# Optimization experiments

Hardware: AMD Instinct MI355X
Metric: run time of the kernel (lower is better)

The kernel has to match this reference:

```python
import jax, jax.numpy as jnp
import numpy as np

N_QUBITS = 8


def _zsign(n):
    # sign of PauliZ eigenvalue for each basis state on each wire; wire 0 is MSB
    idx = np.arange(2 ** n)
    bits = (idx[:, None] >> (n - 1 - np.arange(n))) & 1
    return jnp.asarray(1.0 - 2.0 * bits, dtype=jnp.float32)  # (2^n, n)


ZSIGN = _zsign(N_QUBITS)


def qgate(angles):
    """Simulate: RX(angle_w) per wire (encoder RX + trainable RX already summed,
    since RX(a)RX(b)=RX(a+b)), CNOT chain, then <Z_w> per wire.
    angles: (B, n) real -> (B, n) expectation values in [-1, 1]."""
    B, n = angles.shape
    c = jnp.cos(angles / 2).astype(jnp.complex64)
    s = (-1j * jnp.sin(angles / 2)).astype(jnp.complex64)
    # product state |psi> = kron_w [cos(a/2), -i sin(a/2)], wire 0 = MSB
    state = jnp.ones((B, 1), jnp.complex64)
    for w in range(n):
        qs = jnp.stack([c[:, w], s[:, w]], axis=-1)  # (B, 2)
        state = (state[:, :, None] * qs[:, None, :]).reshape(B, -1)
    # CNOT chain on wires (i, i+1)
    for i in range(n - 1):
        d0, d1 = 2 ** i, 2 ** (n - i - 2)
        st = state.reshape(B, d0, 2, 2, d1)
        st = jnp.stack([st[:, :, 0], st[:, :, 1, ::-1]], axis=2)
        state = st.reshape(B, -1)
    probs = state.real ** 2 + state.imag ** 2  # (B, 2^n)
    return probs @ ZSIGN  # (B, n)


def setup_inputs() -> dict:
    key = jax.random.key(0)
    S, B, D, H = 256, 256, 256, N_QUBITS
    fan = D + H
    ks = jax.random.split(key, 13)
    inputs = jax.random.normal(ks[0], (S, B, D), dtype=jnp.float32)
    hx = jnp.zeros((B, H), jnp.float32)
    cx = jnp.zeros((B, H), jnp.float32)
    bound = 1.0 / np.sqrt(fan)

    def lin(kw, kb):
        W = jax.random.uniform(kw, (H, fan), minval=-bound, maxval=bound, dtype=jnp.float32)
        b = jax.random.uniform(kb, (H,), minval=-bound, maxval=bound, dtype=jnp.float32)
        return W, b

    Wf, bf = lin(ks[1], ks[2])
    Wi, bi = lin(ks[3], ks[4])
    Wu, bu = lin(ks[5], ks[6])
    Wo, bo = lin(ks[7], ks[8])
    theta_f = jax.random.normal(ks[9], (H,), dtype=jnp.float32) * 0.1
    theta_i = jax.random.normal(ks[10], (H,), dtype=jnp.float32) * 0.1
    theta_u = jax.random.normal(ks[11], (H,), dtype=jnp.float32) * 0.1
    theta_o = jax.random.normal(ks[12], (H,), dtype=jnp.float32) * 0.1
    return {"inputs": inputs, "hx": hx, "cx": cx,
            "Wf": Wf, "bf": bf, "Wi": Wi, "bi": bi,
            "Wu": Wu, "bu": bu, "Wo": Wo, "bo": bo,
            "theta_f": theta_f, "theta_i": theta_i,
            "theta_u": theta_u, "theta_o": theta_o}


def reference(inputs, hx, cx, Wf, bf, Wi, bi, Wu, bu, Wo, bo,
              theta_f, theta_i, theta_u, theta_o):
    def step(carry, x):
        h, c = carry
        z = jnp.concatenate([x, h], axis=1)  # (B, D+H)
        f = jax.nn.sigmoid(qgate(z @ Wf.T + bf + theta_f))
        i = jax.nn.sigmoid(qgate(z @ Wi.T + bi + theta_i))
        g = jnp.tanh(qgate(z @ Wu.T + bu + theta_u))
        o = jax.nn.sigmoid(qgate(z @ Wo.T + bo + theta_o))
        c = f * c + i * g
        h = o * jnp.tanh(c)
        return (h, c), h

    (hT, cT), outs = jax.lax.scan(step, (hx, cx), inputs)
    return outs, hT, cT
```

## Files before the change

kernel.cpp:

```cpp
#include <hip/hip_runtime.h>


#define S_LEN 256
#define BATCH 256
#define DIMK  256
#define FAN   264
#define NROWS (S_LEN * BATCH)
#define WS_NEED ((size_t)NROWS * 32 * 4)

typedef __attribute__((address_space(1))) const void GV;
typedef __attribute__((address_space(3))) void LV;

__device__ __forceinline__ float lo16f(unsigned u) {
    union { unsigned u; float f; } v; v.u = u << 16; return v.f;
}
__device__ __forceinline__ float hi16f(unsigned u) {
    union { unsigned u; float f; } v; v.u = u & 0xffff0000u; return v.f;
}
__device__ __forceinline__ float b2f(unsigned short u) {
    union { unsigned u; float f; } v; v.u = ((unsigned)u) << 16; return v.f;
}
__device__ __forceinline__ unsigned short f2b(float f) {
    union { float f; unsigned u; } v; v.f = f;
    unsigned r = v.u + 0x7fffu + ((v.u >> 16) & 1u);
    return (unsigned short)(r >> 16);
}
__device__ __forceinline__ float sane(float x) {
    return (__builtin_fabsf(x) < 1e30f) ? x : 0.f;
}
__device__ __forceinline__ float ldE(const void* p, int idx, bool f32) {
    return f32 ? ((const float*)p)[idx] : b2f(((const unsigned short*)p)[idx]);
}
__device__ __forceinline__ void stE(void* p, long idx, float v, bool f32) {
    if (f32) ((float*)p)[idx] = v;
    else     ((unsigned short*)p)[idx] = f2b(v);
}
__device__ __forceinline__ float sigp(float x) {
    float x2 = x * x;
    float p = fmaf(x2, 0.0026216f, -0.0217557f);
    p = fmaf(x2, p, 0.250193f);
    return fmaf(x, p, 0.5f);
}
__device__ __forceinline__ float tanh_pade(float x) {
    float x2 = x * x;
    float num = x * fmaf(x2, x2 + 105.f, 945.f);
    float den = fmaf(x2, fmaf(x2, 15.f, 420.f), 945.f);
    return __fdividef(num, den);
}
__device__ __forceinline__ float tanh_f(float x) {
    return 1.f - __fdividef(2.f, __expf(2.f * x) + 1.f);
}

template<int CTRL>
__device__ __forceinline__ float dpp_f(float x) {
    int xi = __builtin_bit_cast(int, x);
    int r = __builtin_amdgcn_update_dpp(xi, xi, CTRL, 0xF, 0xF, false);
    return __builtin_bit_cast(float, r);
}
template<int IMM>
__device__ __forceinline__ float swz_f(float x) {
    return __builtin_bit_cast(float,
        __builtin_amdgcn_ds_swizzle(__builtin_bit_cast(int, x), IMM));
}
__device__ __forceinline__ float rdlane_f(float x, int l) {
    return __builtin_bit_cast(float,
        __builtin_amdgcn_readlane(__builtin_bit_cast(int, x), l));
}

__device__ __forceinline__ int sniff_f32(const void* X) {
    const unsigned short* u = (const unsigned short*)X;
    int hits = 0;
    for (int i = 0; i < 64; ++i) {
        int e = (u[2 * i] >> 7) & 0xFF;
        if (e >= 110 && e <= 135) ++hits;
    }
    return (hits < 32) ? 1 : 0;
}

__global__ __launch_bounds__(512, 4) void qlstm_gemm(
    const void* __restrict__ X,
    const void* __restrict__ Wf, const void* __restrict__ Wi,
    const void* __restrict__ Wu, const void* __restrict__ Wo,
    const void* __restrict__ bf_, const void* __restrict__ bi_,
    const void* __restrict__ bu_, const void* __restrict__ bo_,
    const void* __restrict__ tf, const void* __restrict__ ti,
    const void* __restrict__ tu, const void* __restrict__ to_,
    float* __restrict__ A)
{
    __shared__ float Xs[8][32][32];
    __shared__ float red[8][32][32];

    const int tid = threadIdx.x;
    const bool f32 = sniff_f32(X) != 0;

    const int kv = tid >> 6;
    const int l  = tid & 63;
    const int o  = l & 31;
    const int th = l >> 5;
    const int g  = o >> 3, w = o & 7;
    const void* Wg = (g == 0) ? Wf : (g == 1) ? Wi : (g == 2) ? Wu : Wo;
    const void* bg_[4] = { bf_, bi_, bu_, bo_ };
    const void* tg_[4] = { tf, ti, tu, to_ };

    float4 wreg[8];
    if (f32) {
        const float4* wr = (const float4*)((const float*)Wg + w * FAN + kv * 32);
#pragma unroll
        for (int i = 0; i < 8; ++i) wreg[i] = wr[i];
    } else {
        const uint4* wr = (const uint4*)((const unsigned short*)Wg + w * FAN + kv * 32);
#pragma unroll
        for (int i = 0; i < 4; ++i) {
            uint4 wu = wr[i];
            wreg[2 * i + 0] = make_float4(lo16f(wu.x), hi16f(wu.x),
                                          lo16f(wu.y), hi16f(wu.y));
            wreg[2 * i + 1] = make_float4(lo16f(wu.z), hi16f(wu.z),
                                          lo16f(wu.w), hi16f(wu.w));
        }
    }

    const long rowbase = (long)blockIdx.x * 64;

    for (int chunk = 0; chunk < 2; ++chunk) {
        if (f32) {
#pragma unroll
            for (int i = 0; i < 4; ++i) {
                const long row = rowbase + chunk * 32 + i * 8 + (l >> 3);
                const int t = (int)(row & 255), bb = (int)(row >> 8);
                const float* src = (const float*)X
                        + ((long)t * BATCH + bb) * DIMK + kv * 32 + (l & 7) * 4;
                __builtin_amdgcn_global_load_lds((GV*)src,
                        (LV*)&Xs[kv][i * 8][0], 16, 0, 0);
            }
            asm volatile("s_waitcnt vmcnt(0)" ::: "memory");
            for (int j = 0; j < 16; ++j) {
                const int r = th * 16 + j;
                const float4* xv = (const float4*)&Xs[kv][r][0];
                float a0 = 0.f, a1 = 0.f, a2 = 0.f, a3 = 0.f;
#pragma unroll
                for (int i = 0; i < 8; ++i) {
                    float4 xu = xv[i];
                    a0 = fmaf(xu.x, wreg[i].x, a0);
                    a1 = fmaf(xu.y, wreg[i].y, a1);
                    a2 = fmaf(xu.z, wreg[i].z, a2);
                    a3 = fmaf(xu.w, wreg[i].w, a3);
                }
                red[kv][r][o] = (a0 + a1) + (a2 + a3);
            }
        } else {
            for (int j = 0; j < 16; ++j) {
                const int r = th * 16 + j;
                const long row = rowbase + chunk * 32 + r;
                const int t = (int)(row & 255), bb = (int)(row >> 8);
                const uint4* xr = (const uint4*)((const unsigned short*)X
                        + ((long)t * BATCH + bb) * DIMK + kv * 32);
                float a0 = 0.f, a1 = 0.f, a2 = 0.f, a3 = 0.f;
#pragma unroll
                for (int i = 0; i < 4; ++i) {
                    uint4 xu = xr[i];
                    a0 = fmaf(lo16f(xu.x), wreg[2 * i].x, a0);
                    a1 = fmaf(hi16f(xu.x), wreg[2 * i].y, a1);
                    a2 = fmaf(lo16f(xu.y), wreg[2 * i].z, a2);
                    a3 = fmaf(hi16f(xu.y), wreg[2 * i].w, a3);
                    a0 = fmaf(lo16f(xu.z), wreg[2 * i + 1].x, a0);
                    a1 = fmaf(hi16f(xu.z), wreg[2 * i + 1].y, a1);
                    a2 = fmaf(lo16f(xu.w), wreg[2 * i + 1].z, a2);
                    a3 = fmaf(hi16f(xu.w), wreg[2 * i + 1].w, a3);
                }
                red[kv][r][o] = (a0 + a1) + (a2 + a3);
            }
        }
        __syncthreads();
        for (int idx = tid; idx < 32 * 32; idx += 512) {
            const int rl = idx >> 5, oo = idx & 31;
            float s = 0.f;
#pragma unroll
            for (int k = 0; k < 8; ++k) s += red[k][rl][oo];
            const int g2 = oo >> 3, w2 = oo & 7;
            const float bt = sane(ldE(bg_[g2], w2, f32))
                           + sane(ldE(tg_[g2], w2, f32));
            A[(rowbase + chunk * 32 + rl) * 32 + w2 * 4 + g2] = sane(s) + bt;
        }
        __syncthreads();
    }
}

__global__ __launch_bounds__(64) void qlstm_rec(
    const void* __restrict__ X,  const void* __restrict__ hx, const void* __restrict__ cx,
    const void* __restrict__ Wf, const void* __restrict__ Wi,
    const void* __restrict__ Wu, const void* __restrict__ Wo,
    void* __restrict__ out, const float* __restrict__ A)
{
    __shared__ float4 Abuf[2][2048];

    const int tid = threadIdx.x;
    const bool f32 = sniff_f32(X) != 0;

    const int p     = tid & 15;
    const int w     = p & 7;
    const int half  = p >> 3;
    const int bsub  = tid >> 4;
    const int bglob = blockIdx.x * 4 + bsub;

    const void* WgA = half ? Wu : Wf;
    const void* WgB = half ? Wo : Wi;

    float WhA[8], WhB[8];
#pragma unroll
    for (int m = 0; m < 8; ++m) {
        WhA[m] = sane(ldE(WgA, w * FAN + DIMK + (w ^ m), f32));
        WhB[m] = sane(ldE(WgB, w * FAN + DIMK + (w ^ m), f32));
    }
    const float d3 = half ? -0.028402f : 0.f;
    const float d2 = half ?  0.121713f : 0.0026216f;
    const float d1 = half ? -0.331717f : -0.0217557f;
    const float d0 = half ?  1.0f      : 0.250193f;
    const float s0 = half ?  0.f       : 0.5f;

    float h = sane(ldE(hx, bglob * 8 + w, f32));
    float c = sane(ldE(cx, bglob * 8 + w, f32));

    auto cumprod8 = [&](float e) {
        { float v = dpp_f<0x111>(e); e = (w >= 1) ? e * v : e; }
        { float v = dpp_f<0x112>(e); e = (w >= 2) ? e * v : e; }
        { float v = dpp_f<0x114>(e); e = (w >= 4) ? e * v : e; }
        return e;
    };

    const float4* A4 = (const float4*)A;
    const int w2 = tid & 7, bs = (tid >> 3) & 3, tl0 = tid >> 5;
    const float4* srcb = A4
        + ((((long)(blockIdx.x * 4 + bs)) << 8 | tl0) << 3) + w2;
    auto stage = [&](int ch, int bufi) {
        const float4* s0p = srcb + ((long)ch << 9);
#pragma unroll
        for (int i = 0; i < 32; ++i) {
            __builtin_amdgcn_global_load_lds((GV*)(s0p + (i << 4)),
                                             (LV*)&Abuf[bufi][i << 6], 16, 0, 0);
        }
    };

    auto STEP = [&](int t, float aA, float aB) {
        float h0 = h;
        float h1 = dpp_f<0xB1>(h);
        float h2 = dpp_f<0x4E>(h);
        float h3 = dpp_f<0xB1>(h2);
        float h7 = dpp_f<0x141>(h);
        float h6 = dpp_f<0xB1>(h7);
        float h5 = dpp_f<0x4E>(h7);
        float h4 = dpp_f<0xB1>(h5);

        float e0, e1;
        {
            float a = fmaf(h0, WhA[0], aA), b = h1 * WhA[1];
            a = fmaf(h2, WhA[2], a); b = fmaf(h3, WhA[3], b);
            a = fmaf(h4, WhA[4], a); b = fmaf(h5, WhA[5], b);
            a = fmaf(h6, WhA[6], a); b = fmaf(h7, WhA[7], b);
            e0 = a + b;
            a = fmaf(h0, WhB[0], aB); b = h1 * WhB[1];
            a = fmaf(h2, WhB[2], a); b = fmaf(h3, WhB[3], b);
            a = fmaf(h4, WhB[4], a); b = fmaf(h5, WhB[5], b);
            a = fmaf(h6, WhB[6], a); b = fmaf(h7, WhB[7], b);
            e1 = a + b;
        }
        float EA = cumprod8(__cosf(e0));
        float EB = cumprod8(__cosf(e1));
        float x2 = EA * EA;
        float pp = fmaf(x2, d3, d2);
        pp = fmaf(x2, pp, d1);
        pp = fmaf(x2, pp, d0);
        float vA = fmaf(EA, pp, s0);
        float vB = sigp(EB);
        float rA = dpp_f<0x128>(vA);
        float rB = dpp_f<0x128>(vB);
        float vf = half ? rA : vA;
        float vi = half ? rB : vB;
        float vu = half ? vA : rA;
        float vo = half ? vB : rB;
        c = fmaf(vf, c, vi * vu);
        h = vo * tanh_pade(c);
        if (half == 0)
            stE(out, (long)t * 2048 + bglob * 8 + w, h, f32);
    };

    stage(0, 0);
    asm volatile("s_waitcnt vmcnt(0)" ::: "memory");

    const float2* Ab2 = (const float2*)&Abuf[0][0];
    const int rdbase = (bsub * 8 + w) * 2 + half;
    for (int ch = 0; ch < 4; ++ch) {
        const int cb = ch & 1;
        if (ch + 1 < 4) stage(ch + 1, cb ^ 1);
#pragma unroll 4
        for (int s = 0; s < 64; ++s) {
            float2 a = Ab2[cb * 4096 + s * 64 + rdbase];
            STEP(ch * 64 + s, a.x, a.y);
        }
        asm volatile("s_waitcnt vmcnt(0)" ::: "memory");
    }
    if (half == 0) {
        stE(out, 524288L + bglob * 8 + w, h, f32);
        stE(out, 526336L + bglob * 8 + w, c, f32);
    }
}

__global__ __launch_bounds__(320, 1) void qlstm_fused_v6(
    const void* __restrict__ X,  const void* __restrict__ hx, const void* __restrict__ cx,
    const void* __restrict__ Wf, const void* __restrict__ bf_,
    const void* __restrict__ Wi, const void* __restrict__ bi_,
    const void* __restrict__ Wu, const void* __restrict__ bu_,
    const void* __restrict__ Wo, const void* __restrict__ bo_,
    const void* __restrict__ tf, const void* __restrict__ ti,
    const void* __restrict__ tu, const void* __restrict__ to_,
    void* __restrict__ out)
{
    __shared__ float As4[2][4][32][32];

    const int tid = threadIdx.x;
    const int b   = blockIdx.x;
    const bool f32 = sniff_f32(X) != 0;

    const int wv   = tid >> 6;
    const int lane = tid & 63;
    const int kv   = wv - 1;
    const int o    = lane & 31;
    const int th   = lane >> 5;
    const int g    = o >> 3, w = o & 7;
    const void* Wg = (g == 0) ? Wf : (g == 1) ? Wi : (g == 2) ? Wu : Wo;

    float4 wreg[16];
    if (wv >= 1) {
        if (f32) {
            const float4* wr = (const float4*)((const float*)Wg + w * FAN + kv * 64);
#pragma unroll
            for (int i = 0; i < 16; ++i) wreg[i] = wr[i];
        } else {
            const uint4* wr = (const uint4*)((const unsigned short*)Wg + w * FAN + kv * 64);
#pragma unroll
            for (int i = 0; i < 8; ++i) {
                uint4 wu = wr[i];
                wreg[2 * i + 0] = make_float4(lo16f(wu.x), hi16f(wu.x),
                                              lo16f(wu.y), hi16f(wu.y));
                wreg[2 * i + 1] = make_float4(lo16f(wu.z), hi16f(wu.z),
                                              lo16f(wu.w), hi16f(wu.w));
            }
        }
    }

    auto fill = [&](int ch) {
        float (*dst)[32] = As4[ch & 1][kv];
        const int tb = ch * 32 + th * 16;
        if (f32) {
            for (int j = 0; j < 16; ++j) {
                const float4* xr = (const float4*)((const float*)X
                        + ((long)(tb + j) * BATCH + b) * DIMK + kv * 64);
                float a0 = 0.f, a1 = 0.f, a2 = 0.f, a3 = 0.f;
#pragma unroll
                for (int i = 0; i < 16; ++i) {
                    float4 xu = xr[i];
                    a0 = fmaf(xu.x, wreg[i].x, a0);
                    a1 = fmaf(xu.y, wreg[i].y, a1);
                    a2 = fmaf(xu.z, wreg[i].z, a2);
                    a3 = fmaf(xu.w, wreg[i].w, a3);
                }
                dst[th * 16 + j][o] = sane((a0 + a1) + (a2 + a3));
            }
        } else {
            for (int j = 0; j < 16; ++j) {
                const uint4* xr = (const uint4*)((const unsigned short*)X
                        + ((long)(tb + j) * BATCH + b) * DIMK + kv * 64);
                float a0 = 0.f, a1 = 0.f, a2 = 0.f, a3 = 0.f;
#pragma unroll
                for (int i = 0; i < 8; ++i) {
                    uint4 xu = xr[i];
                    a0 = fmaf(lo16f(xu.x), wreg[2 * i].x, a0);
                    a1 = fmaf(hi16f(xu.x), wreg[2 * i].y, a1);
                    a2 = fmaf(lo16f(xu.y), wreg[2 * i].z, a2);
                    a3 = fmaf(hi16f(xu.y), wreg[2 * i].w, a3);
                    a0 = fmaf(lo16f(xu.z), wreg[2 * i + 1].x, a0);
                    a1 = fmaf(hi16f(xu.z), wreg[2 * i + 1].y, a1);
                    a2 = fmaf(lo16f(xu.w), wreg[2 * i + 1].z, a2);
                    a3 = fmaf(hi16f(xu.w), wreg[2 * i + 1].w, a3);
                }
                dst[th * 16 + j][o] = sane((a0 + a1) + (a2 + a3));
            }
        }
    };

    float Wh[8];
    float bt = 0.f, h = 0.f, c = 0.f, qv = 1.f;
    int rw = 0, rg = 0;
    if (tid < 32) {
        rw = tid & 7; rg = tid >> 3;
        const void* bg = (rg == 0) ? bf_ : (rg == 1) ? bi_ : (rg == 2) ? bu_ : bo_;
        const void* tg = (rg == 0) ? tf  : (rg == 1) ? ti  : (rg == 2) ? tu  : to_;
        const int wr = rw * FAN;
#pragma unroll
        for (int j = 0; j < 8; ++j)
            Wh[j] = sane(ldE(Wg, wr + DIMK + j, f32));
        bt = sane(ldE(bg, rw, f32)) + sane(ldE(tg, rw, f32));
        h  = sane(ldE(hx, b * 8 + rw, f32));
        c  = sane(ldE(cx, b * 8 + rw, f32));
        qv = (rg == 2) ? 2.f : 1.f;
    }
    if (wv == 0) __builtin_amdgcn_s_setprio(1);

    if (wv >= 1) fill(0);
    __syncthreads();

    for (int ch = 0; ch < 8; ++ch) {
        if (wv >= 1 && ch + 1 < 8) fill(ch + 1);
        if (tid < 32) {
            const int buf = ch & 1;
            float n0 = As4[buf][0][0][tid], n1 = As4[buf][1][0][tid];
            float n2 = As4[buf][2][0][tid], n3 = As4[buf][3][0][tid];
            float a_cur = (n0 + n1) + (n2 + n3);
            for (int s = 0; s < 32; ++s) {
                const int sn = (s < 31) ? s + 1 : s;
                float m0 = As4[buf][0][sn][tid], m1 = As4[buf][1][sn][tid];
                float m2 = As4[buf][2][sn][tid], m3 = As4[buf][3][sn][tid];
                float dd0 = 0.f, dd1 = 0.f;
#pragma unroll
                for (int j = 0; j < 8; j += 2) {
                    dd0 = fmaf(rdlane_f(h, j),     Wh[j],     dd0);
                    dd1 = fmaf(rdlane_f(h, j + 1), Wh[j + 1], dd1);
                }
                float ang = a_cur + bt + (dd0 + dd1);
                float e = __cosf(ang);
                { float v = dpp_f<0x111>(e); e = (rw >= 1) ? e * v : e; }
                { float v = dpp_f<0x112>(e); e = (rw >= 2) ? e * v : e; }
                { float v = dpp_f<0x114>(e); e = (rw >= 4) ? e * v : e; }
                float ez  = __expf(qv * e);
                float val = 1.f - __fdividef(qv, ez + 1.f);
                float fg = swz_f<0x007>(val);
                float ig = swz_f<0x107>(val);
                float ug = swz_f<0x207>(val);
                float og = swz_f<0x307>(val);
                c = fmaf(fg, c, ig * ug);
                float e2 = __expf(2.f * c);
                float th2 = 1.f - __fdividef(2.f, e2 + 1.f);
                h = og * th2;
                if (rg == 0)
                    stE(out, (long)(ch * 32 + s) * 2048 + b * 8 + rw, h, f32);
                a_cur = (m0 + m1) + (m2 + m3);
            }
        }
        __syncthreads();
    }

    if (tid < 32 && rg == 0) {
        stE(out, 524288L + b * 8 + rw, h, f32);
        stE(out, 526336L + b * 8 + rw, c, f32);
    }
}

extern "C" void kernel_launch(void* const* d_in, const int* in_sizes, int n_in,
                              void* d_out, int out_size, void* d_ws, size_t ws_size,
                              hipStream_t stream) {
    if (d_ws != nullptr && ws_size >= WS_NEED) {
        qlstm_gemm<<<dim3(NROWS / 64), dim3(512), 0, stream>>>(
            d_in[0], d_in[3], d_in[5], d_in[7], d_in[9],
            d_in[4], d_in[6], d_in[8], d_in[10],
            d_in[11], d_in[12], d_in[13], d_in[14],
            (float*)d_ws);
        qlstm_rec<<<dim3(BATCH / 4), dim3(64), 0, stream>>>(
            d_in[0], d_in[1], d_in[2],
            d_in[3], d_in[5], d_in[7], d_in[9],
            d_out, (const float*)d_ws);
    } else {
        qlstm_fused_v6<<<dim3(BATCH), dim3(320), 0, stream>>>(
            d_in[0], d_in[1], d_in[2],
            d_in[3], d_in[4], d_in[5], d_in[6],
            d_in[7], d_in[8], d_in[9], d_in[10],
            d_in[11], d_in[12], d_in[13], d_in[14],
            d_out);
    }
}
```

Measured before the change: 207.2 us.

## Restructure gemm register tiling and split recurrent gates across lanes

The input-projection GEMM now holds all four gate weight slices in registers per thread, so each X row loaded from LDS is reused across the four gates, and both chunks are staged up front as a double buffer. The recurrent kernel assigns one gate per lane (2 batches per wave instead of 4) and exchanges gate values through DPP and ds_swizzle, which halves the per-lane serial work in each time step and doubles the number of blocks. The cost is higher register pressure in the GEMM (its occupancy hint drops from 4 to 2) and extra cross-lane shuffles in the recurrence.

```diff
diff --git a/kernel.cpp b/kernel.cpp
--- a/kernel.cpp
+++ b/kernel.cpp
@@ -35,20 +35,20 @@
     if (f32) ((float*)p)[idx] = v;
     else     ((unsigned short*)p)[idx] = f2b(v);
 }
+__device__ __forceinline__ float tanh_pade(float x) {
+    float x2 = x * x;
+    float num = x * fmaf(x2, x2 + 105.f, 945.f);
+    float den = fmaf(x2, fmaf(x2, 15.f, 420.f), 945.f);
+    return __fdividef(num, den);
+}
+__device__ __forceinline__ float tanh_f(float x) {
+    return 1.f - __fdividef(2.f, __expf(2.f * x) + 1.f);
+}
 __device__ __forceinline__ float sigp(float x) {
     float x2 = x * x;
     float p = fmaf(x2, 0.0026216f, -0.0217557f);
     p = fmaf(x2, p, 0.250193f);
     return fmaf(x, p, 0.5f);
-}
-__device__ __forceinline__ float tanh_pade(float x) {
-    float x2 = x * x;
-    float num = x * fmaf(x2, x2 + 105.f, 945.f);
-    float den = fmaf(x2, fmaf(x2, 15.f, 420.f), 945.f);
-    return __fdividef(num, den);
-}
-__device__ __forceinline__ float tanh_f(float x) {
-    return 1.f - __fdividef(2.f, __expf(2.f * x) + 1.f);
 }
 
 template<int CTRL>
@@ -77,7 +77,7 @@
     return (hits < 32) ? 1 : 0;
 }
 
-__global__ __launch_bounds__(512, 4) void qlstm_gemm(
+__global__ __launch_bounds__(512, 2) void qlstm_gemm(
     const void* __restrict__ X,
     const void* __restrict__ Wf, const void* __restrict__ Wi,
     const void* __restrict__ Wu, const void* __restrict__ Wo,
@@ -87,90 +87,75 @@
     const void* __restrict__ tu, const void* __restrict__ to_,
     float* __restrict__ A)
 {
-    __shared__ float Xs[8][32][32];
+    __shared__ float Xs[2][8][32][32];
     __shared__ float red[8][32][32];
 
     const int tid = threadIdx.x;
     const bool f32 = sniff_f32(X) != 0;
 
-    const int kv = tid >> 6;
-    const int l  = tid & 63;
-    const int o  = l & 31;
-    const int th = l >> 5;
-    const int g  = o >> 3, w = o & 7;
-    const void* Wg = (g == 0) ? Wf : (g == 1) ? Wi : (g == 2) ? Wu : Wo;
+    const int kv  = tid >> 6;
+    const int l   = tid & 63;
+    const int o4  = l & 7;
+    const int rg8 = l >> 3;
+    const void* Wq[4] = { Wf, Wi, Wu, Wo };
     const void* bg_[4] = { bf_, bi_, bu_, bo_ };
     const void* tg_[4] = { tf, ti, tu, to_ };
 
-    float4 wreg[8];
-    if (f32) {
-        const float4* wr = (const float4*)((const float*)Wg + w * FAN + kv * 32);
-#pragma unroll
-        for (int i = 0; i < 8; ++i) wreg[i] = wr[i];
-    } else {
-        const uint4* wr = (const uint4*)((const unsigned short*)Wg + w * FAN + kv * 32);
+    float4 wregQ[4][8];
+#pragma unroll
+    for (int q = 0; q < 4; ++q) {
+        if (f32) {
+            const float4* wr = (const float4*)((const float*)Wq[q] + o4 * FAN + kv * 32);
+#pragma unroll
+            for (int i = 0; i < 8; ++i) wregQ[q][i] = wr[i];
+        } else {
+            const uint4* wr = (const uint4*)((const unsigned short*)Wq[q] + o4 * FAN + kv * 32);
+#pragma unroll
+            for (int i = 0; i < 4; ++i) {
+                uint4 wu = wr[i];
+                wregQ[q][2 * i + 0] = make_float4(lo16f(wu.x), hi16f(wu.x),
+                                                  lo16f(wu.y), hi16f(wu.y));
+                wregQ[q][2 * i + 1] = make_float4(lo16f(wu.z), hi16f(wu.z),
+                                                  lo16f(wu.w), hi16f(wu.w));
+            }
+        }
+    }
+
+    const long rowbase = (long)blockIdx.x * 64;
+
+    auto stageX = [&](int chunk, int cbuf) {
 #pragma unroll
         for (int i = 0; i < 4; ++i) {
-            uint4 wu = wr[i];
-            wreg[2 * i + 0] = make_float4(lo16f(wu.x), hi16f(wu.x),
-                                          lo16f(wu.y), hi16f(wu.y));
-            wreg[2 * i + 1] = make_float4(lo16f(wu.z), hi16f(wu.z),
-                                          lo16f(wu.w), hi16f(wu.w));
-        }
-    }
-
-    const long rowbase = (long)blockIdx.x * 64;
-
-    for (int chunk = 0; chunk < 2; ++chunk) {
-        if (f32) {
-#pragma unroll
-            for (int i = 0; i < 4; ++i) {
-                const long row = rowbase + chunk * 32 + i * 8 + (l >> 3);
-                const int t = (int)(row & 255), bb = (int)(row >> 8);
-                const float* src = (const float*)X
-                        + ((long)t * BATCH + bb) * DIMK + kv * 32 + (l & 7) * 4;
-                __builtin_amdgcn_global_load_lds((GV*)src,
-                        (LV*)&Xs[kv][i * 8][0], 16, 0, 0);
-            }
-            asm volatile("s_waitcnt vmcnt(0)" ::: "memory");
-            for (int j = 0; j < 16; ++j) {
-                const int r = th * 16 + j;
-                const float4* xv = (const float4*)&Xs[kv][r][0];
+            const long row = rowbase + chunk * 32 + i * 8 + (l >> 3);
+            const int t = (int)(row & 255), bb = (int)(row >> 8);
+            const float* src = (const float*)X
+                    + ((long)t * BATCH + bb) * DIMK + kv * 32 + (l & 7) * 4;
+            __builtin_amdgcn_global_load_lds((GV*)src,
+                    (LV*)&Xs[cbuf][kv][i * 8][0], 16, 0, 0);
+        }
+    };
+    auto computeChunk = [&](int cbuf) {
+        for (int j = 0; j < 4; ++j) {
+            const int r = rg8 * 4 + j;
+            const float4* xv = (const float4*)&Xs[cbuf][kv][r][0];
+            float4 x8[8];
+#pragma unroll
+            for (int i = 0; i < 8; ++i) x8[i] = xv[i];
+#pragma unroll
+            for (int q = 0; q < 4; ++q) {
                 float a0 = 0.f, a1 = 0.f, a2 = 0.f, a3 = 0.f;
 #pragma unroll
                 for (int i = 0; i < 8; ++i) {
-                    float4 xu = xv[i];
-                    a0 = fmaf(xu.x, wreg[i].x, a0);
-                    a1 = fmaf(xu.y, wreg[i].y, a1);
-                    a2 = fmaf(xu.z, wreg[i].z, a2);
-                    a3 = fmaf(xu.w, wreg[i].w, a3);
+                    a0 = fmaf(x8[i].x, wregQ[q][i].x, a0);
+                    a1 = fmaf(x8[i].y, wregQ[q][i].y, a1);
+                    a2 = fmaf(x8[i].z, wregQ[q][i].z, a2);
+                    a3 = fmaf(x8[i].w, wregQ[q][i].w, a3);
                 }
-                red[kv][r][o] = (a0 + a1) + (a2 + a3);
-            }
-        } else {
-            for (int j = 0; j < 16; ++j) {
-                const int r = th * 16 + j;
-                const long row = rowbase + chunk * 32 + r;
-                const int t = (int)(row & 255), bb = (int)(row >> 8);
-                const uint4* xr = (const uint4*)((const unsigned short*)X
-                        + ((long)t * BATCH + bb) * DIMK + kv * 32);
-                float a0 = 0.f, a1 = 0.f, a2 = 0.f, a3 = 0.f;
-#pragma unroll
-                for (int i = 0; i < 4; ++i) {
-                    uint4 xu = xr[i];
-                    a0 = fmaf(lo16f(xu.x), wreg[2 * i].x, a0);
-                    a1 = fmaf(hi16f(xu.x), wreg[2 * i].y, a1);
-                    a2 = fmaf(lo16f(xu.y), wreg[2 * i].z, a2);
-                    a3 = fmaf(hi16f(xu.y), wreg[2 * i].w, a3);
-                    a0 = fmaf(lo16f(xu.z), wreg[2 * i + 1].x, a0);
-                    a1 = fmaf(hi16f(xu.z), wreg[2 * i + 1].y, a1);
-                    a2 = fmaf(lo16f(xu.w), wreg[2 * i + 1].z, a2);
-                    a3 = fmaf(hi16f(xu.w), wreg[2 * i + 1].w, a3);
-                }
-                red[kv][r][o] = (a0 + a1) + (a2 + a3);
-            }
-        }
-        __syncthreads();
+                red[kv][r][q * 8 + o4] = (a0 + a1) + (a2 + a3);
+            }
+        }
+    };
+    auto reduceWrite = [&](int chunk) {
         for (int idx = tid; idx < 32 * 32; idx += 512) {
             const int rl = idx >> 5, oo = idx & 31;
             float s = 0.f;
@@ -181,7 +166,56 @@
                            + sane(ldE(tg_[g2], w2, f32));
             A[(rowbase + chunk * 32 + rl) * 32 + w2 * 4 + g2] = sane(s) + bt;
         }
+    };
+
+    if (f32) {
+        stageX(0, 0);
+        stageX(1, 1);
+        asm volatile("s_waitcnt vmcnt(4)" ::: "memory");
+        computeChunk(0);
         __syncthreads();
+        reduceWrite(0);
+        __syncthreads();
+        asm volatile("s_waitcnt vmcnt(0)" ::: "memory");
+        computeChunk(1);
+        __syncthreads();
+        reduceWrite(1);
+    } else {
+        for (int chunk = 0; chunk < 2; ++chunk) {
+            for (int j = 0; j < 4; ++j) {
+                const int r = rg8 * 4 + j;
+                const long row = rowbase + chunk * 32 + r;
+                const int t = (int)(row & 255), bb = (int)(row >> 8);
+                const uint4* xr = (const uint4*)((const unsigned short*)X
+                        + ((long)t * BATCH + bb) * DIMK + kv * 32);
+                uint4 xu[4];
+#pragma unroll
+                for (int i = 0; i < 4; ++i) xu[i] = xr[i];
+                float4 x8[8];
+#pragma unroll
+                for (int i = 0; i < 4; ++i) {
+                    x8[2 * i + 0] = make_float4(lo16f(xu[i].x), hi16f(xu[i].x),
+                                                lo16f(xu[i].y), hi16f(xu[i].y));
+                    x8[2 * i + 1] = make_float4(lo16f(xu[i].z), hi16f(xu[i].z),
+                                                lo16f(xu[i].w), hi16f(xu[i].w));
+                }
+#pragma unroll
+                for (int q = 0; q < 4; ++q) {
+                    float a0 = 0.f, a1 = 0.f, a2 = 0.f, a3 = 0.f;
+#pragma unroll
+                    for (int i = 0; i < 8; ++i) {
+                        a0 = fmaf(x8[i].x, wregQ[q][i].x, a0);
+                        a1 = fmaf(x8[i].y, wregQ[q][i].y, a1);
+                        a2 = fmaf(x8[i].z, wregQ[q][i].z, a2);
+                        a3 = fmaf(x8[i].w, wregQ[q][i].w, a3);
+                    }
+                    red[kv][r][q * 8 + o4] = (a0 + a1) + (a2 + a3);
+                }
+            }
+            __syncthreads();
+            reduceWrite(chunk);
+            __syncthreads();
+        }
     }
 }
 
@@ -191,31 +225,30 @@
     const void* __restrict__ Wu, const void* __restrict__ Wo,
     void* __restrict__ out, const float* __restrict__ A)
 {
-    __shared__ float4 Abuf[2][2048];
+    __shared__ float4 Abuf[2][1024];
 
     const int tid = threadIdx.x;
     const bool f32 = sniff_f32(X) != 0;
 
-    const int p     = tid & 15;
-    const int w     = p & 7;
-    const int half  = p >> 3;
-    const int bsub  = tid >> 4;
-    const int bglob = blockIdx.x * 4 + bsub;
-
-    const void* WgA = half ? Wu : Wf;
-    const void* WgB = half ? Wo : Wi;
-
-    float WhA[8], WhB[8];
-#pragma unroll
-    for (int m = 0; m < 8; ++m) {
-        WhA[m] = sane(ldE(WgA, w * FAN + DIMK + (w ^ m), f32));
-        WhB[m] = sane(ldE(WgB, w * FAN + DIMK + (w ^ m), f32));
-    }
-    const float d3 = half ? -0.028402f : 0.f;
-    const float d2 = half ?  0.121713f : 0.0026216f;
-    const float d1 = half ? -0.331717f : -0.0217557f;
-    const float d0 = half ?  1.0f      : 0.250193f;
-    const float s0 = half ?  0.f       : 0.5f;
+    const int p  = tid & 31;
+    const int g  = p >> 3;
+    const int w  = p & 7;
+    const int b2 = tid >> 5;
+    const int bglob = blockIdx.x * 2 + b2;
+    const bool gb0 = (g & 1) != 0, gb1 = (g & 2) != 0;
+
+    const void* Wg = (g == 0) ? Wf : (g == 1) ? Wi : (g == 2) ? Wu : Wo;
+
+    float Whm[8];
+#pragma unroll
+    for (int m = 0; m < 8; ++m)
+        Whm[m] = sane(ldE(Wg, w * FAN + DIMK + (w ^ m), f32));
+
+    const float d3 = (g == 2) ? -0.028402f : 0.f;
+    const float d2 = (g == 2) ?  0.121713f : 0.0026216f;
+    const float d1 = (g == 2) ? -0.331717f : -0.0217557f;
+    const float d0 = (g == 2) ?  1.0f      : 0.250193f;
+    const float s0 = (g == 2) ?  0.f       : 0.5f;
 
     float h = sane(ldE(hx, bglob * 8 + w, f32));
     float c = sane(ldE(cx, bglob * 8 + w, f32));
@@ -228,19 +261,17 @@
     };
 
     const float4* A4 = (const float4*)A;
-    const int w2 = tid & 7, bs = (tid >> 3) & 3, tl0 = tid >> 5;
-    const float4* srcb = A4
-        + ((((long)(blockIdx.x * 4 + bs)) << 8 | tl0) << 3) + w2;
+    const float4* srcbase = A4 + (long)blockIdx.x * 4096;
     auto stage = [&](int ch, int bufi) {
-        const float4* s0p = srcb + ((long)ch << 9);
-#pragma unroll
-        for (int i = 0; i < 32; ++i) {
-            __builtin_amdgcn_global_load_lds((GV*)(s0p + (i << 4)),
-                                             (LV*)&Abuf[bufi][i << 6], 16, 0, 0);
-        }
-    };
-
-    auto STEP = [&](int t, float aA, float aB) {
+#pragma unroll
+        for (int i = 0; i < 16; ++i) {
+            const float4* s = srcbase + ch * 512 + i * 64 + tid + (i >= 8 ? 1536 : 0);
+            __builtin_amdgcn_global_load_lds((GV*)s,
+                    (LV*)&Abuf[bufi][i * 64], 16, 0, 0);
+        }
+    };
+
+    auto STEP = [&](int t, float a) {
         float h0 = h;
         float h1 = dpp_f<0xB1>(h);
         float h2 = dpp_f<0x4E>(h);
@@ -250,55 +281,53 @@
         float h5 = dpp_f<0x4E>(h7);
         float h4 = dpp_f<0xB1>(h5);
 
-        float e0, e1;
-        {
-            float a = fmaf(h0, WhA[0], aA), b = h1 * WhA[1];
-            a = fmaf(h2, WhA[2], a); b = fmaf(h3, WhA[3], b);
-            a = fmaf(h4, WhA[4], a); b = fmaf(h5, WhA[5], b);
-            a = fmaf(h6, WhA[6], a); b = fmaf(h7, WhA[7], b);
-            e0 = a + b;
-            a = fmaf(h0, WhB[0], aB); b = h1 * WhB[1];
-            a = fmaf(h2, WhB[2], a); b = fmaf(h3, WhB[3], b);
-            a = fmaf(h4, WhB[4], a); b = fmaf(h5, WhB[5], b);
-            a = fmaf(h6, WhB[6], a); b = fmaf(h7, WhB[7], b);
-            e1 = a + b;
-        }
-        float EA = cumprod8(__cosf(e0));
-        float EB = cumprod8(__cosf(e1));
-        float x2 = EA * EA;
+        float da = fmaf(h0, Whm[0], a), db = h1 * Whm[1];
+        da = fmaf(h2, Whm[2], da); db = fmaf(h3, Whm[3], db);
+        da = fmaf(h4, Whm[4], da); db = fmaf(h5, Whm[5], db);
+        da = fmaf(h6, Whm[6], da); db = fmaf(h7, Whm[7], db);
+        float ang = da + db;
+
+        float E = cumprod8(__cosf(ang));
+        float x2 = E * E;
         float pp = fmaf(x2, d3, d2);
         pp = fmaf(x2, pp, d1);
         pp = fmaf(x2, pp, d0);
-        float vA = fmaf(EA, pp, s0);
-        float vB = sigp(EB);
-        float rA = dpp_f<0x128>(vA);
-        float rB = dpp_f<0x128>(vB);
-        float vf = half ? rA : vA;
-        float vi = half ? rB : vB;
-        float vu = half ? vA : rA;
-        float vo = half ? vB : rB;
-        c = fmaf(vf, c, vi * vu);
-        h = vo * tanh_pade(c);
-        if (half == 0)
+        float v = fmaf(E, pp, s0);
+
+        float v8  = dpp_f<0x128>(v);
+        float v16 = swz_f<0x401F>(v);
+        float v24 = swz_f<0x401F>(v8);
+        float fa = gb0 ? v8  : v;
+        float fb = gb0 ? v24 : v16;
+        float ia = gb0 ? v   : v8;
+        float ib = gb0 ? v16 : v24;
+        float gf = gb1 ? fb : fa;
+        float gu = gb1 ? fa : fb;
+        float gi = gb1 ? ib : ia;
+        float go = gb1 ? ia : ib;
+
+        c = fmaf(gf, c, gi * gu);
+        h = go * tanh_pade(c);
+        if (g == 0)
             stE(out, (long)t * 2048 + bglob * 8 + w, h, f32);
     };
 
     stage(0, 0);
     asm volatile("s_waitcnt vmcnt(0)" ::: "memory");
 
-    const float2* Ab2 = (const float2*)&Abuf[0][0];
-    const int rdbase = (bsub * 8 + w) * 2 + half;
+    const float* Afl = (const float*)&Abuf[0][0];
+    const int rdoff = b2 * 2048 + w * 4 + g;
     for (int ch = 0; ch < 4; ++ch) {
         const int cb = ch & 1;
         if (ch + 1 < 4) stage(ch + 1, cb ^ 1);
 #pragma unroll 4
         for (int s = 0; s < 64; ++s) {
-            float2 a = Ab2[cb * 4096 + s * 64 + rdbase];
-            STEP(ch * 64 + s, a.x, a.y);
+            float a = Afl[cb * 4096 + s * 32 + rdoff];
+            STEP(ch * 64 + s, a);
         }
         asm volatile("s_waitcnt vmcnt(0)" ::: "memory");
     }
-    if (half == 0) {
+    if (g == 0) {
         stE(out, 524288L + bglob * 8 + w, h, f32);
         stE(out, 526336L + bglob * 8 + w, c, f32);
     }
@@ -463,7 +492,7 @@
             d_in[4], d_in[6], d_in[8], d_in[10],
             d_in[11], d_in[12], d_in[13], d_in[14],
             (float*)d_ws);
-        qlstm_rec<<<dim3(BATCH / 4), dim3(64), 0, stream>>>(
+        qlstm_rec<<<dim3(BATCH / 2), dim3(64), 0, stream>>>(
             d_in[0], d_in[1], d_in[2],
             d_in[3], d_in[5], d_in[7], d_in[9],
             d_out, (const float*)d_ws);
```

Result: slower. 214.7 us (+3.6%).
